# Performance work log

Hardware: AMD Instinct MI355X
Metric: run time of the kernel (lower is better)

Reference implementation:

```python
import jax, jax.numpy as jnp
import numpy as np

C_IN, C_OUT, ORDER, BATCH, N = 4, 8, 3, 8, 512
STDV = 1.0 / 3.0


def setup_inputs() -> dict:
    key = jax.random.key(0)
    k0, k1, k2, k3, k4 = jax.random.split(key, 5)
    s_in = jax.random.normal(k0, (C_IN, BATCH, N, N), dtype=jnp.float32)
    a_o = jax.random.normal(k1, (BATCH, N, N), dtype=jnp.float32)
    alpha = jax.random.normal(k2, (C_OUT, C_IN), dtype=jnp.float32) * STDV + 1.0
    beta = jax.random.normal(k3, (C_OUT, C_IN), dtype=jnp.float32) * STDV + 0.0
    coeffs = jax.random.normal(k4, (C_OUT, ORDER + 1, C_IN), dtype=jnp.float32) * STDV
    coeffs = coeffs.at[:, 1, :].set(1.0)  # torch init sets linear Cheb coeff to 1
    tau = jnp.linspace(0.01, 0.9, C_OUT).astype(jnp.float32).reshape(C_OUT, 1, 1, 1)
    return {"s_in": s_in, "a_o": a_o, "alpha": alpha, "beta": beta,
            "coeffs": coeffs, "tau": tau}


def _cheb_terms(A, n_terms):
    # Chebyshev matrix polynomial basis: T0=I, T1=A, T_k = 2*A@T_{k-1} - T_{k-2}
    b, n, _ = A.shape
    terms = [jnp.broadcast_to(jnp.eye(n, dtype=A.dtype), (b, n, n)), A]
    for _ in range(2, n_terms):
        terms.append(2.0 * jnp.matmul(A, terms[-1]) - terms[-2])
    return jnp.stack(terms[:n_terms])  # (n_terms, b, n, n)


def reference(s_in, a_o, alpha, beta, coeffs, tau):
    # s_in: (c_in, B, N, N); a_o: (B, N, N)
    c_out, n_terms, c_in = coeffs.shape
    n = a_o.shape[-1]
    # mimo_tensor_polynomial with cob='cheb': a_o is identical across c_in,
    # so compute the Cheb basis once on (B,N,N) and contract with coeffs.
    T = _cheb_terms(a_o, n_terms)                      # (K+1, B, N, N)
    poly = jnp.einsum('oki,kbnm->oibnm', coeffs, T)    # (c_out, c_in, B, N, N)
    # a@a_o + a_o@a is independent of c_out (broadcast in torch), compute once
    mix = jnp.matmul(s_in, a_o) + jnp.matmul(a_o, s_in)  # (c_in, B, N, N)
    temp = (alpha[:, :, None, None, None] * s_in
            + beta[:, :, None, None, None] * mix
            + poly)                                     # (c_out, c_in, B, N, N)
    zd = 1.0 - jnp.eye(n, dtype=temp.dtype)             # zero diagonal mask
    temp = temp * zd
    temp = jnp.mean(temp, axis=1)                       # (c_out, B, N, N)
    # normalize_slices(which_norm='max_abs'): per (c_out, batch) slice
    mx = jnp.max(jnp.abs(temp), axis=(-2, -1), keepdims=True)
    temp = temp / jnp.where(mx == 0, jnp.ones_like(mx), mx)
    return jax.nn.relu(temp - tau)
```

## Files before the change

kernel.cpp:

```cpp
#include <hip/hip_runtime.h>

#define NDIM 512
#define NN (512*512)

typedef float          fv4  __attribute__((ext_vector_type(4)));
typedef unsigned int   uv2  __attribute__((ext_vector_type(2)));
typedef unsigned int   uv4  __attribute__((ext_vector_type(4)));
typedef unsigned short usv4 __attribute__((ext_vector_type(4)));
typedef unsigned short usv8 __attribute__((ext_vector_type(8)));
typedef short          sv8  __attribute__((ext_vector_type(8)));

__device__ __forceinline__ unsigned short f2bf(float x){
    unsigned u = __builtin_bit_cast(unsigned, x);
    u += 0x7fffu + ((u >> 16) & 1u);
    return (unsigned short)(u >> 16);
}
__device__ __forceinline__ float bf2f(unsigned short s){
    unsigned u = ((unsigned)s) << 16;
    return __builtin_bit_cast(float, u);
}

#define MFMA16(acc, va, vb) \
    acc = __builtin_amdgcn_mfma_f32_16x16x32_bf16( \
        __builtin_bit_cast(sv8, va), __builtin_bit_cast(sv8, vb), acc, 0, 0, 0)

#define TRREAD(dst, addr) \
    asm volatile("ds_read_b64_tr_b16 %0, %1" : "=v"(dst) : "v"(addr))

__global__ __launch_bounds__(256) void preconv_kernel(
    const float* __restrict__ s_in, const float* __restrict__ a_o,
    unsigned short* __restrict__ s_bf, unsigned short* __restrict__ Ah,
    unsigned short* __restrict__ Al)
{
    const int z  = blockIdx.y;
    const int e0 = blockIdx.x * 1024 + threadIdx.x * 4;
    if (z < 32) {
        float4 v = *(const float4*)(s_in + z * NN + e0);
        float vv[4] = {v.x, v.y, v.z, v.w};
        usv4 o;
        #pragma unroll
        for (int j = 0; j < 4; ++j) o[j] = f2bf(vv[j]);
        *(usv4*)(s_bf + z * NN + e0) = o;
    } else {
        const int b = z - 32;
        float4 v = *(const float4*)(a_o + b * NN + e0);
        float vv[4] = {v.x, v.y, v.z, v.w};
        usv4 h, l;
        #pragma unroll
        for (int j = 0; j < 4; ++j) {
            unsigned short hb = f2bf(vv[j]);
            h[j] = hb;
            l[j] = f2bf(vv[j] - bf2f(hb));
        }
        *(usv4*)(Ah + b * NN + e0) = h;
        *(usv4*)(Al + b * NN + e0) = l;
    }
}

__global__ __launch_bounds__(256) void gemm_fused_kernel(
    const unsigned short* __restrict__ s_bf,
    const unsigned short* __restrict__ Ah, const unsigned short* __restrict__ Al,
    unsigned short* __restrict__ AAh, unsigned short* __restrict__ AAl,
    float* __restrict__ AA, float* __restrict__ AAA,
    unsigned short* __restrict__ MIXbf, int stage)
{
    const int z = blockIdx.z;
    const bool split = (stage == 0) || (z < 8);

    const unsigned short *X1, *X2, *Y1, *Y2;
    if (stage == 0)      { X1 = Ah + z * NN;  X2 = Al + z * NN;
                           Y1 = Ah + z * NN;  Y2 = Al + z * NN; }
    else if (z < 8)      { X1 = Ah + z * NN;  X2 = Al + z * NN;
                           Y1 = AAh + z * NN; Y2 = AAl + z * NN; }
    else                 { const int z2 = z - 8, b = z2 & 7;
                           X1 = s_bf + z2 * NN; X2 = Ah + b * NN;
                           Y1 = Ah + b * NN;    Y2 = s_bf + z2 * NN; }

    const int row0 = blockIdx.y * 128, col0 = blockIdx.x * 128;
    const int tid = threadIdx.x, lane = tid & 63, w = tid >> 6;

    __shared__ unsigned short Xa[2][128][40], Xb[2][128][40];
    __shared__ unsigned short Ba[2][4096], Bb[2][4096];

    fv4 acc[4][4];
    #pragma unroll
    for (int mi = 0; mi < 4; ++mi)
        #pragma unroll
        for (int ni = 0; ni < 4; ++ni) acc[mi][ni] = (fv4)0.f;

    const int xr  = tid >> 2, xc = (tid & 3) << 3;
    const int xo0 = (row0 + xr) * NDIM + xc;
    const int xo1 = xo0 + 64 * NDIM;
    const int kl = tid & 3, hh = (tid >> 2) & 1, cs = (tid >> 3) & 7, kh = tid >> 6;
    const int kb0 = kh * 4 + kl;
    const int yo0 = kb0 * NDIM + col0 + cs * 16 + hh * 8;
    const int yo1 = yo0 + 16 * NDIM;
    const int lb0 = cs * 512 + kb0 * 16 + hh * 8;
    const int lb1 = lb0 + 256;

    const unsigned laneoff = (((unsigned)lane >> 4) << 7) | (((unsigned)lane & 15) << 3);
    const unsigned wcol    = ((unsigned)(w & 1)) << 12;
    const int g4 = (lane >> 4) * 4;

    usv8 lx1a, lx1b, lx2a, lx2b, ly1a, ly1b, ly2a, ly2b;

    auto gload = [&](int k0) {
        lx1a = *(const usv8*)(X1 + xo0 + k0);
        lx1b = *(const usv8*)(X1 + xo1 + k0);
        lx2a = *(const usv8*)(X2 + xo0 + k0);
        lx2b = *(const usv8*)(X2 + xo1 + k0);
        ly1a = *(const usv8*)(Y1 + yo0 + k0 * NDIM);
        ly1b = *(const usv8*)(Y1 + yo1 + k0 * NDIM);
        ly2a = *(const usv8*)(Y2 + yo0 + k0 * NDIM);
        ly2b = *(const usv8*)(Y2 + yo1 + k0 * NDIM);
    };
    auto swrite = [&](int buf) {
        *(usv8*)&Xa[buf][xr][xc]      = lx1a;
        *(usv8*)&Xa[buf][64 + xr][xc] = lx1b;
        *(usv8*)&Xb[buf][xr][xc]      = lx2a;
        *(usv8*)&Xb[buf][64 + xr][xc] = lx2b;
        *(usv8*)&Ba[buf][lb0] = ly1a;
        *(usv8*)&Ba[buf][lb1] = ly1b;
        *(usv8*)&Bb[buf][lb0] = ly2a;
        *(usv8*)&Bb[buf][lb1] = ly2b;
    };
    auto compute = [&](int buf) {
        const unsigned ba_base = (unsigned)(uintptr_t)&Ba[buf][0];
        const unsigned bb_base = (unsigned)(uintptr_t)&Bb[buf][0];
        uv2 fa[4][2], fb[4][2];
        #pragma unroll
        for (int ni = 0; ni < 4; ++ni)
            #pragma unroll
            for (int h = 0; h < 2; ++h) {
                TRREAD(fa[ni][h], ba_base + wcol + laneoff + ni * 1024 + h * 512);
                TRREAD(fb[ni][h], bb_base + wcol + laneoff + ni * 1024 + h * 512);
            }
        asm volatile("s_waitcnt lgkmcnt(0)" ::: "memory");
        __builtin_amdgcn_sched_barrier(0);

        #pragma unroll
        for (int mi = 0; mi < 4; ++mi) {
            const unsigned short* xr1 = &Xa[buf][(w >> 1) * 64 + mi * 16 + (lane & 15)][0];
            const unsigned short* xr2 = &Xb[buf][(w >> 1) * 64 + mi * 16 + (lane & 15)][0];
            uv2 a0 = *(const uv2*)(xr1 + g4);
            uv2 a1 = *(const uv2*)(xr1 + 16 + g4);
            uv2 b0 = *(const uv2*)(xr2 + g4);
            uv2 b1 = *(const uv2*)(xr2 + 16 + g4);
            uv4 xva = {a0.x, a0.y, a1.x, a1.y};
            uv4 xvb = {b0.x, b0.y, b1.x, b1.y};
            #pragma unroll
            for (int ni = 0; ni < 4; ++ni) {
                uv4 vba = {fa[ni][0].x, fa[ni][0].y, fa[ni][1].x, fa[ni][1].y};
                uv4 vbb = {fb[ni][0].x, fb[ni][0].y, fb[ni][1].x, fb[ni][1].y};
                if (split) {
                    MFMA16(acc[mi][ni], xva, vba);
                    MFMA16(acc[mi][ni], xva, vbb);
                    MFMA16(acc[mi][ni], xvb, vba);
                } else {
                    MFMA16(acc[mi][ni], xva, vba);
                    MFMA16(acc[mi][ni], xvb, vbb);
                }
            }
        }
    };

    gload(0);
    swrite(0);
    __syncthreads();
    int cur = 0;
    for (int t = 0; t < 15; ++t) {
        gload((t + 1) * 32);
        compute(cur);
        swrite(cur ^ 1);
        __syncthreads();
        cur ^= 1;
    }
    compute(cur);

    const int g = lane >> 4, c15 = lane & 15;
    if (split) {
        float* C = (stage == 0) ? (AA + z * NN) : (AAA + z * NN);
        #pragma unroll
        for (int mi = 0; mi < 4; ++mi)
            #pragma unroll
            for (int ni = 0; ni < 4; ++ni) {
                int r = row0 + (w >> 1) * 64 + mi * 16 + g * 4;
                int c = col0 + (w & 1) * 64 + ni * 16 + c15;
                #pragma unroll
                for (int q = 0; q < 4; ++q) {
                    float v = acc[mi][ni][q];
                    C[(r + q) * NDIM + c] = v;
                    if (stage == 0) {
                        unsigned short hb = f2bf(v);
                        AAh[z * NN + (r + q) * NDIM + c] = hb;
                        AAl[z * NN + (r + q) * NDIM + c] = f2bf(v - bf2f(hb));
                    }
                }
            }
    } else {
        unsigned short* Cm = MIXbf + (z - 8) * NN;
        #pragma unroll
        for (int mi = 0; mi < 4; ++mi)
            #pragma unroll
            for (int ni = 0; ni < 4; ++ni) {
                int r = row0 + (w >> 1) * 64 + mi * 16 + g * 4;
                int c = col0 + (w & 1) * 64 + ni * 16 + c15;
                #pragma unroll
                for (int q = 0; q < 4; ++q)
                    Cm[(r + q) * NDIM + c] = f2bf(acc[mi][ni][q]);
            }
    }
}

__global__ __launch_bounds__(256) void combine_kernel(
    const unsigned short* __restrict__ s_bf, const unsigned short* __restrict__ Ah,
    const float* __restrict__ AA, const float* __restrict__ AAA,
    const unsigned short* __restrict__ MIXbf,
    const float* __restrict__ alpha, const float* __restrict__ beta,
    const float* __restrict__ coeffs,
    float* __restrict__ out, unsigned short* __restrict__ tmp,
    unsigned int* __restrict__ smax, int use_tmp)
{
    const int b  = blockIdx.y;
    const int e0 = blockIdx.x * 2048 + threadIdx.x * 8;
    const int n  = e0 >> 9;
    const int m0 = e0 & 511;

    float ca[8], cb[8], cc[8];
    #pragma unroll
    for (int o = 0; o < 8; ++o) {
        float c1 = 0.f, c2 = 0.f, c3 = 0.f;
        #pragma unroll
        for (int i = 0; i < 4; ++i) {
            c1 += coeffs[o * 16 + 4 + i];
            c2 += coeffs[o * 16 + 8 + i];
            c3 += coeffs[o * 16 + 12 + i];
        }
        ca[o] = c1 - 3.f * c3; cb[o] = 2.f * c2; cc[o] = 4.f * c3;
    }

    float av[8], aav[8], aaav[8], sv[4][8], mv[4][8];
    {
        usv8 a8 = *(const usv8*)(Ah + b * NN + e0);
        #pragma unroll
        for (int j = 0; j < 8; ++j) av[j] = bf2f(a8[j]);
        const float4 q0 = *(const float4*)(AA + b * NN + e0);
        const float4 q1 = *(const float4*)(AA + b * NN + e0 + 4);
        aav[0]=q0.x; aav[1]=q0.y; aav[2]=q0.z; aav[3]=q0.w;
        aav[4]=q1.x; aav[5]=q1.y; aav[6]=q1.z; aav[7]=q1.w;
        const float4 r0 = *(const float4*)(AAA + b * NN + e0);
        const float4 r1 = *(const float4*)(AAA + b * NN + e0 + 4);
        aaav[0]=r0.x; aaav[1]=r0.y; aaav[2]=r0.z; aaav[3]=r0.w;
        aaav[4]=r1.x; aaav[5]=r1.y; aaav[6]=r1.z; aaav[7]=r1.w;
        #pragma unroll
        for (int i = 0; i < 4; ++i) {
            usv8 s8 = *(const usv8*)(s_bf + (i * 8 + b) * NN + e0);
            usv8 m8 = *(const usv8*)(MIXbf + (i * 8 + b) * NN + e0);
            #pragma unroll
            for (int j = 0; j < 8; ++j) { sv[i][j] = bf2f(s8[j]); mv[i][j] = bf2f(m8[j]); }
        }
    }

    float lmax[8];
    #pragma unroll
    for (int o = 0; o < 8; ++o) {
        float outv[8];
        float lm = 0.f;
        #pragma unroll
        for (int j = 0; j < 8; ++j) {
            float t = ca[o] * av[j] + cb[o] * aav[j] + cc[o] * aaav[j];
            #pragma unroll
            for (int i = 0; i < 4; ++i)
                t += alpha[o * 4 + i] * sv[i][j] + beta[o * 4 + i] * mv[i][j];
            t *= 0.25f;
            if (n == m0 + j) t = 0.f;
            outv[j] = t;
            lm = fmaxf(lm, fabsf(t));
        }
        lmax[o] = lm;
        if (use_tmp) {
            usv8 ov;
            #pragma unroll
            for (int j = 0; j < 8; ++j) ov[j] = f2bf(outv[j]);
            *(usv8*)(tmp + (o * 8 + b) * NN + e0) = ov;
        } else {
            *(float4*)(out + (o * 8 + b) * NN + e0) =
                make_float4(outv[0], outv[1], outv[2], outv[3]);
            *(float4*)(out + (o * 8 + b) * NN + e0 + 4) =
                make_float4(outv[4], outv[5], outv[6], outv[7]);
        }
    }

    #pragma unroll
    for (int o = 0; o < 8; ++o) {
        #pragma unroll
        for (int off = 32; off > 0; off >>= 1)
            lmax[o] = fmaxf(lmax[o], __shfl_xor(lmax[o], off, 64));
    }
    __shared__ float red[4][8];
    const int lane = threadIdx.x & 63, wv = threadIdx.x >> 6;
    if (lane == 0) {
        #pragma unroll
        for (int o = 0; o < 8; ++o) red[wv][o] = lmax[o];
    }
    __syncthreads();
    if (threadIdx.x < 8) {
        const int o = threadIdx.x;
        const float mfin = fmaxf(fmaxf(red[0][o], red[1][o]), fmaxf(red[2][o], red[3][o]));
        atomicMax(&smax[o * 8 + b], __float_as_uint(mfin));
    }
}

__global__ __launch_bounds__(256) void norm_kernel(
    float* __restrict__ out, const unsigned short* __restrict__ tmp,
    const unsigned int* __restrict__ smax, const float* __restrict__ tau,
    int use_tmp)
{
    const int ob = blockIdx.y;
    const float mx = __uint_as_float(smax[ob]);
    const float inv = (mx == 0.f) ? 1.f : (1.f / mx);
    const float t = tau[ob >> 3];
    const int e0 = blockIdx.x * 2048 + threadIdx.x * 8;
    float v[8];
    if (use_tmp) {
        usv8 tv = *(const usv8*)(tmp + ob * NN + e0);
        #pragma unroll
        for (int j = 0; j < 8; ++j) v[j] = bf2f(tv[j]);
    } else {
        float4 v0 = *(float4*)(out + ob * NN + e0);
        float4 v1 = *(float4*)(out + ob * NN + e0 + 4);
        v[0]=v0.x; v[1]=v0.y; v[2]=v0.z; v[3]=v0.w;
        v[4]=v1.x; v[5]=v1.y; v[6]=v1.z; v[7]=v1.w;
    }
    #pragma unroll
    for (int j = 0; j < 8; ++j) v[j] = fmaxf(fmaf(v[j], inv, -t), 0.f);
    *(float4*)(out + ob * NN + e0)     = make_float4(v[0], v[1], v[2], v[3]);
    *(float4*)(out + ob * NN + e0 + 4) = make_float4(v[4], v[5], v[6], v[7]);
}

extern "C" void kernel_launch(void* const* d_in, const int* in_sizes, int n_in,
                              void* d_out, int out_size, void* d_ws, size_t ws_size,
                              hipStream_t stream) {
    (void)in_sizes; (void)n_in; (void)out_size;
    const float* s_in   = (const float*)d_in[0];
    const float* a_o    = (const float*)d_in[1];
    const float* alpha  = (const float*)d_in[2];
    const float* beta   = (const float*)d_in[3];
    const float* coeffs = (const float*)d_in[4];
    const float* tau    = (const float*)d_in[5];
    float* out = (float*)d_out;

    float* AA  = (float*)d_ws;
    float* AAA = AA + 8 * NN;
    unsigned short* s_bf  = (unsigned short*)(AAA + 8 * NN);
    unsigned short* Ah    = s_bf + 32 * NN;
    unsigned short* Al    = Ah + 8 * NN;
    unsigned short* AAh   = Al + 8 * NN;
    unsigned short* AAl   = AAh + 8 * NN;
    unsigned short* MIXbf = AAl + 8 * NN;
    unsigned int* SMAX = (unsigned int*)(MIXbf + 32 * NN);
    unsigned short* TMP = (unsigned short*)(SMAX + 64);

    const size_t need_tmp = (size_t)((char*)(TMP + 64 * NN) - (char*)d_ws);
    const int use_tmp = (ws_size >= need_tmp) ? 1 : 0;

    hipLaunchKernelGGL(preconv_kernel, dim3(256, 40), dim3(256), 0, stream,
                       s_in, a_o, s_bf, Ah, Al);
    hipLaunchKernelGGL(gemm_fused_kernel, dim3(4, 4, 8), dim3(256), 0, stream,
                       s_bf, Ah, Al, AAh, AAl, AA, AAA, MIXbf, 0);
    hipLaunchKernelGGL(gemm_fused_kernel, dim3(4, 4, 40), dim3(256), 0, stream,
                       s_bf, Ah, Al, AAh, AAl, AA, AAA, MIXbf, 1);
    hipMemsetAsync(SMAX, 0, 64 * sizeof(unsigned int), stream);
    hipLaunchKernelGGL(combine_kernel, dim3(128, 8), dim3(256), 0, stream,
                       s_bf, Ah, AA, AAA, MIXbf, alpha, beta, coeffs,
                       out, TMP, SMAX, use_tmp);
    hipLaunchKernelGGL(norm_kernel, dim3(128, 64), dim3(256), 0, stream,
                       out, TMP, SMAX, tau, use_tmp);
}
```

Before: 225.9 us.

## Use 512-thread GEMM blocks with 8 waves sharing each 128x128 tile

The fused GEMM kernel now runs with 512 threads per block instead of 256. Each of the 8 waves computes a 32x64 sub-tile instead of 64x64, and each thread loads half as many global vectors per k-step. The goal is more waves per CU to hide latency, since the grid is small (128 and 640 blocks). In exchange, each wave issues more LDS B-fragment reads relative to its MFMA work, since every wave still reads the full B fragments for its column half.

Measured after the change: 213.5 us. 1.06x faster.

```diff
diff --git a/kernel.cpp b/kernel.cpp
--- a/kernel.cpp
+++ b/kernel.cpp
@@ -57,7 +57,7 @@
     }
 }
 
-__global__ __launch_bounds__(256) void gemm_fused_kernel(
+__global__ __launch_bounds__(512) void gemm_fused_kernel(
     const unsigned short* __restrict__ s_bf,
     const unsigned short* __restrict__ Ah, const unsigned short* __restrict__ Al,
     unsigned short* __restrict__ AAh, unsigned short* __restrict__ AAl,
@@ -78,51 +78,42 @@
 
     const int row0 = blockIdx.y * 128, col0 = blockIdx.x * 128;
     const int tid = threadIdx.x, lane = tid & 63, w = tid >> 6;
+    const int wr = w >> 1, wc = w & 1;
 
     __shared__ unsigned short Xa[2][128][40], Xb[2][128][40];
     __shared__ unsigned short Ba[2][4096], Bb[2][4096];
 
-    fv4 acc[4][4];
-    #pragma unroll
-    for (int mi = 0; mi < 4; ++mi)
+    fv4 acc[2][4];
+    #pragma unroll
+    for (int mi = 0; mi < 2; ++mi)
         #pragma unroll
         for (int ni = 0; ni < 4; ++ni) acc[mi][ni] = (fv4)0.f;
 
     const int xr  = tid >> 2, xc = (tid & 3) << 3;
-    const int xo0 = (row0 + xr) * NDIM + xc;
-    const int xo1 = xo0 + 64 * NDIM;
-    const int kl = tid & 3, hh = (tid >> 2) & 1, cs = (tid >> 3) & 7, kh = tid >> 6;
-    const int kb0 = kh * 4 + kl;
-    const int yo0 = kb0 * NDIM + col0 + cs * 16 + hh * 8;
-    const int yo1 = yo0 + 16 * NDIM;
-    const int lb0 = cs * 512 + kb0 * 16 + hh * 8;
-    const int lb1 = lb0 + 256;
+    const int xo  = (row0 + xr) * NDIM + xc;
+    const int kl = tid & 3, hh = (tid >> 2) & 1, cs = (tid >> 3) & 7,
+              kh = (tid >> 6) & 7;
+    const int kb  = kh * 4 + kl;
+    const int yo  = kb * NDIM + col0 + cs * 16 + hh * 8;
+    const int lb  = cs * 512 + kb * 16 + hh * 8;
 
     const unsigned laneoff = (((unsigned)lane >> 4) << 7) | (((unsigned)lane & 15) << 3);
-    const unsigned wcol    = ((unsigned)(w & 1)) << 12;
+    const unsigned wcol    = ((unsigned)wc) << 12;
     const int g4 = (lane >> 4) * 4;
 
-    usv8 lx1a, lx1b, lx2a, lx2b, ly1a, ly1b, ly2a, ly2b;
+    usv8 lx1, lx2, ly1, ly2;
 
     auto gload = [&](int k0) {
-        lx1a = *(const usv8*)(X1 + xo0 + k0);
-        lx1b = *(const usv8*)(X1 + xo1 + k0);
-        lx2a = *(const usv8*)(X2 + xo0 + k0);
-        lx2b = *(const usv8*)(X2 + xo1 + k0);
-        ly1a = *(const usv8*)(Y1 + yo0 + k0 * NDIM);
-        ly1b = *(const usv8*)(Y1 + yo1 + k0 * NDIM);
-        ly2a = *(const usv8*)(Y2 + yo0 + k0 * NDIM);
-        ly2b = *(const usv8*)(Y2 + yo1 + k0 * NDIM);
+        lx1 = *(const usv8*)(X1 + xo + k0);
+        lx2 = *(const usv8*)(X2 + xo + k0);
+        ly1 = *(const usv8*)(Y1 + yo + k0 * NDIM);
+        ly2 = *(const usv8*)(Y2 + yo + k0 * NDIM);
     };
     auto swrite = [&](int buf) {
-        *(usv8*)&Xa[buf][xr][xc]      = lx1a;
-        *(usv8*)&Xa[buf][64 + xr][xc] = lx1b;
-        *(usv8*)&Xb[buf][xr][xc]      = lx2a;
-        *(usv8*)&Xb[buf][64 + xr][xc] = lx2b;
-        *(usv8*)&Ba[buf][lb0] = ly1a;
-        *(usv8*)&Ba[buf][lb1] = ly1b;
-        *(usv8*)&Bb[buf][lb0] = ly2a;
-        *(usv8*)&Bb[buf][lb1] = ly2b;
+        *(usv8*)&Xa[buf][xr][xc] = lx1;
+        *(usv8*)&Xb[buf][xr][xc] = lx2;
+        *(usv8*)&Ba[buf][lb] = ly1;
+        *(usv8*)&Bb[buf][lb] = ly2;
     };
     auto compute = [&](int buf) {
         const unsigned ba_base = (unsigned)(uintptr_t)&Ba[buf][0];
@@ -139,9 +130,9 @@
         __builtin_amdgcn_sched_barrier(0);
 
         #pragma unroll
-        for (int mi = 0; mi < 4; ++mi) {
-            const unsigned short* xr1 = &Xa[buf][(w >> 1) * 64 + mi * 16 + (lane & 15)][0];
-            const unsigned short* xr2 = &Xb[buf][(w >> 1) * 64 + mi * 16 + (lane & 15)][0];
+        for (int mi = 0; mi < 2; ++mi) {
+            const unsigned short* xr1 = &Xa[buf][wr * 32 + mi * 16 + (lane & 15)][0];
+            const unsigned short* xr2 = &Xb[buf][wr * 32 + mi * 16 + (lane & 15)][0];
             uv2 a0 = *(const uv2*)(xr1 + g4);
             uv2 a1 = *(const uv2*)(xr1 + 16 + g4);
             uv2 b0 = *(const uv2*)(xr2 + g4);
@@ -181,11 +172,11 @@
     if (split) {
         float* C = (stage == 0) ? (AA + z * NN) : (AAA + z * NN);
         #pragma unroll
-        for (int mi = 0; mi < 4; ++mi)
+        for (int mi = 0; mi < 2; ++mi)
             #pragma unroll
             for (int ni = 0; ni < 4; ++ni) {
-                int r = row0 + (w >> 1) * 64 + mi * 16 + g * 4;
-                int c = col0 + (w & 1) * 64 + ni * 16 + c15;
+                int r = row0 + wr * 32 + mi * 16 + g * 4;
+                int c = col0 + wc * 64 + ni * 16 + c15;
                 #pragma unroll
                 for (int q = 0; q < 4; ++q) {
                     float v = acc[mi][ni][q];
@@ -200,11 +191,11 @@
     } else {
         unsigned short* Cm = MIXbf + (z - 8) * NN;
         #pragma unroll
-        for (int mi = 0; mi < 4; ++mi)
+        for (int mi = 0; mi < 2; ++mi)
             #pragma unroll
             for (int ni = 0; ni < 4; ++ni) {
-                int r = row0 + (w >> 1) * 64 + mi * 16 + g * 4;
-                int c = col0 + (w & 1) * 64 + ni * 16 + c15;
+                int r = row0 + wr * 32 + mi * 16 + g * 4;
+                int c = col0 + wc * 64 + ni * 16 + c15;
                 #pragma unroll
                 for (int q = 0; q < 4; ++q)
                     Cm[(r + q) * NDIM + c] = f2bf(acc[mi][ni][q]);
@@ -366,9 +357,9 @@
 
     hipLaunchKernelGGL(preconv_kernel, dim3(256, 40), dim3(256), 0, stream,
                        s_in, a_o, s_bf, Ah, Al);
-    hipLaunchKernelGGL(gemm_fused_kernel, dim3(4, 4, 8), dim3(256), 0, stream,
+    hipLaunchKernelGGL(gemm_fused_kernel, dim3(4, 4, 8), dim3(512), 0, stream,
                        s_bf, Ah, Al, AAh, AAl, AA, AAA, MIXbf, 0);
-    hipLaunchKernelGGL(gemm_fused_kernel, dim3(4, 4, 40), dim3(256), 0, stream,
+    hipLaunchKernelGGL(gemm_fused_kernel, dim3(4, 4, 40), dim3(512), 0, stream,
                        s_bf, Ah, Al, AAh, AAl, AA, AAA, MIXbf, 1);
     hipMemsetAsync(SMAX, 0, 64 * sizeof(unsigned int), stream);
     hipLaunchKernelGGL(combine_kernel, dim3(128, 8), dim3(256), 0, stream,
```
